# Optimization experiments

Hardware: AMD Instinct MI355X
Metric: run time of the kernel (lower is better)

Reference implementation:

```python
import jax, jax.numpy as jnp
import numpy as np

N_NODES = 100000
N_EDGES = 3200000
N_FEAT = 512
N_CLASS = 10
HIDDEN = 16
EPS = 1e-12  # matches torch F.normalize clamp


def setup_inputs() -> dict:
    key = jax.random.key(0)
    ks = jax.random.split(key, 6)
    x = jax.random.normal(ks[0], (N_NODES, N_FEAT), dtype=jnp.float32)
    edge_index = jax.random.randint(ks[1], (2, N_EDGES), 0, N_NODES, dtype=jnp.int64)
    W1 = jax.random.normal(ks[2], (N_FEAT, HIDDEN), dtype=jnp.float32) / np.sqrt(N_FEAT)
    b1 = jnp.zeros((HIDDEN,), dtype=jnp.float32)
    beta = jnp.ones((1,), dtype=jnp.float32)  # learnable scalar of prop2
    W2 = jax.random.normal(ks[3], (HIDDEN, N_CLASS), dtype=jnp.float32) / np.sqrt(HIDDEN)
    b2 = jnp.zeros((N_CLASS,), dtype=jnp.float32)
    return {"x": x, "edge_index": edge_index, "W1": W1, "b1": b1,
            "beta": beta, "W2": W2, "b2": b2}


def _agnn_conv(h, src, dst, beta_val, n_nodes):
    # L2-normalize node features (cosine attention)
    norm = jnp.maximum(jnp.linalg.norm(h, axis=-1, keepdims=True), EPS)
    hn = h / norm
    # per-edge attention logit: beta * cos(h_i, h_j)
    alpha = beta_val * jnp.sum(hn[src] * hn[dst], axis=-1)  # [E]
    # scatter-softmax over edges sharing the same destination node
    amax = jax.ops.segment_max(alpha, dst, num_segments=n_nodes)
    ea = jnp.exp(alpha - amax[dst])
    denom = jax.ops.segment_sum(ea, dst, num_segments=n_nodes)
    w = ea / denom[dst]  # self-loops guarantee denom > 0
    # weighted aggregation of source features into destination nodes
    return jax.ops.segment_sum(w[:, None] * h[src], dst, num_segments=n_nodes)


def reference(x, edge_index, W1, b1, beta, W2, b2):
    n = x.shape[0]
    # dropout is identity in eval mode
    h = jax.nn.relu(x @ W1 + b1)  # [N, 16]
    # AGNNConv adds self-loops before propagation
    loops = jnp.arange(n, dtype=edge_index.dtype)
    src = jnp.concatenate([edge_index[0], loops])
    dst = jnp.concatenate([edge_index[1], loops])
    h = _agnn_conv(h, src, dst, jnp.float32(1.0), n)   # prop1: beta fixed to 1
    h = _agnn_conv(h, src, dst, beta[0], n)            # prop2: learnable beta
    logits = h @ W2 + b2
    return jax.nn.log_softmax(logits, axis=-1)
```

## Files before the change

kernel.cpp:

```cpp
#include <hip/hip_runtime.h>
#include <hip/hip_fp16.h>
#include <math.h>

#define N_NODES 100000
#define N_EDGES 3200000
#define EPRIME  (N_EDGES + N_NODES)
#define NFEAT   512
#define HID     16
#define NCLS    10

#define NPB     256
#define NB      ((N_NODES + NPB - 1) / NPB)
#define CHUNK   4096
#define NCH     ((EPRIME + CHUNK - 1) / CHUNK)
#define CAPB    10240

union U2 { unsigned int u; __half2 h; };
__device__ __forceinline__ float2 u2f(unsigned int v) {
  U2 t; t.u = v; return __half22float2(t.h);
}

__global__ __launch_bounds__(256) void k_gemm_norm(const float* __restrict__ x,
                                                   const float* __restrict__ W1,
                                                   const float* __restrict__ b1,
                                                   __half* __restrict__ hn1,
                                                   float* __restrict__ norms1,
                                                   int* __restrict__ gcur) {
  if (blockIdx.x == 0)
    for (int i = threadIdx.x; i < NB; i += 256) gcur[i] = 0;

  const int lane = threadIdx.x & 63;
  const int wid  = blockIdx.x * 4 + (threadIdx.x >> 6);
  const int nw   = gridDim.x * 4;

  float4 w[8][4];
#pragma unroll
  for (int kk = 0; kk < 8; ++kk)
#pragma unroll
    for (int j = 0; j < 4; ++j)
      w[kk][j] = *reinterpret_cast<const float4*>(W1 + (lane * 8 + kk) * 16 + j * 4);

  const int outCol = (lane >> 2) & 15;
  const float bias = b1[outCol];

  const float4 z4 = make_float4(0.f, 0.f, 0.f, 0.f);
  float4 c0 = z4, c1 = z4, p0 = z4, p1 = z4, t0 = z4, t1 = z4;

  if (wid < N_NODES) {
    c0 = *reinterpret_cast<const float4*>(x + (size_t)wid * NFEAT + lane * 8);
    c1 = *reinterpret_cast<const float4*>(x + (size_t)wid * NFEAT + lane * 8 + 4);
  }
  if (wid + nw < N_NODES) {
    p0 = *reinterpret_cast<const float4*>(x + (size_t)(wid + nw) * NFEAT + lane * 8);
    p1 = *reinterpret_cast<const float4*>(x + (size_t)(wid + nw) * NFEAT + lane * 8 + 4);
  }

  for (int row = wid; row < N_NODES; row += nw) {
    const int r2 = row + 2 * nw;
    if (r2 < N_NODES) {
      t0 = *reinterpret_cast<const float4*>(x + (size_t)r2 * NFEAT + lane * 8);
      t1 = *reinterpret_cast<const float4*>(x + (size_t)r2 * NFEAT + lane * 8 + 4);
    }

    float xs[8] = {c0.x, c0.y, c0.z, c0.w, c1.x, c1.y, c1.z, c1.w};

    float acc[16];
#pragma unroll
    for (int j = 0; j < 16; ++j) acc[j] = 0.f;

#pragma unroll
    for (int kk = 0; kk < 8; ++kk) {
      const float xv = xs[kk];
#pragma unroll
      for (int j4 = 0; j4 < 4; ++j4) {
        acc[j4 * 4 + 0] = fmaf(xv, w[kk][j4].x, acc[j4 * 4 + 0]);
        acc[j4 * 4 + 1] = fmaf(xv, w[kk][j4].y, acc[j4 * 4 + 1]);
        acc[j4 * 4 + 2] = fmaf(xv, w[kk][j4].z, acc[j4 * 4 + 2]);
        acc[j4 * 4 + 3] = fmaf(xv, w[kk][j4].w, acc[j4 * 4 + 3]);
      }
    }

#pragma unroll
    for (int i = 0; i < 8; ++i) {
      float send = (lane & 32) ? acc[i] : acc[i + 8];
      float r = __shfl_xor(send, 32);
      acc[i] = ((lane & 32) ? acc[i + 8] : acc[i]) + r;
    }
#pragma unroll
    for (int i = 0; i < 4; ++i) {
      float send = (lane & 16) ? acc[i] : acc[i + 4];
      float r = __shfl_xor(send, 16);
      acc[i] = ((lane & 16) ? acc[i + 4] : acc[i]) + r;
    }
#pragma unroll
    for (int i = 0; i < 2; ++i) {
      float send = (lane & 8) ? acc[i] : acc[i + 2];
      float r = __shfl_xor(send, 8);
      acc[i] = ((lane & 8) ? acc[i + 2] : acc[i]) + r;
    }
    {
      float send = (lane & 4) ? acc[0] : acc[1];
      float r = __shfl_xor(send, 4);
      acc[0] = ((lane & 4) ? acc[1] : acc[0]) + r;
    }
    acc[0] += __shfl_xor(acc[0], 2);
    acc[0] += __shfl_xor(acc[0], 1);

    const float v = fmaxf(acc[0] + bias, 0.f);
    float ss = v * v;
    ss += __shfl_xor(ss, 4);
    ss += __shfl_xor(ss, 8);
    ss += __shfl_xor(ss, 16);
    ss += __shfl_xor(ss, 32);
    const float nrm = sqrtf(ss);
    const float vs = v / fmaxf(nrm, 1e-12f);

    const float wv = __shfl(vs, (lane & 15) * 4);
    if (lane < 16) hn1[(size_t)row * HID + lane] = __float2half_rn(wv);
    if (lane == 0) norms1[row] = nrm;

    c0 = p0; c1 = p1; p0 = t0; p1 = t1;
  }
}

__global__ __launch_bounds__(256) void k_part(const int* __restrict__ ei,
                                              int* __restrict__ gcur,
                                              unsigned int* __restrict__ slots) {
  __shared__ int sh_hist[NB];
  __shared__ int sh_gbase[NB];
  const int tid = threadIdx.x;

  for (int i = tid; i < NB; i += 256) sh_hist[i] = 0;
  __syncthreads();

  const int base = blockIdx.x * CHUNK;
  unsigned int pk[16];
  int bk[16], rk[16];
#pragma unroll
  for (int j = 0; j < 16; ++j) {
    int e = base + j * 256 + tid;
    bool valid = (e < EPRIME);
    int srcv = 0, d = 0;
    if (valid) {
      if (e < N_EDGES) { srcv = ei[e]; d = ei[N_EDGES + e]; }
      else             { srcv = d = e - N_EDGES; }
    }
    bk[j] = valid ? (d >> 8) : -1;
    pk[j] = (unsigned)srcv | ((unsigned)(d & 255) << 20);
    rk[j] = valid ? atomicAdd(&sh_hist[d >> 8], 1) : 0;
  }
  __syncthreads();

  for (int i = tid; i < NB; i += 256) {
    int hc = sh_hist[i];
    sh_gbase[i] = hc ? atomicAdd(&gcur[i], hc) : 0;
  }
  __syncthreads();

#pragma unroll
  for (int j = 0; j < 16; ++j)
    if (bk[j] >= 0)
      slots[(size_t)bk[j] * CAPB + sh_gbase[bk[j]] + rk[j]] = pk[j];
}

__global__ __launch_bounds__(256) void k_csr(const unsigned int* __restrict__ slots,
                                             const int* __restrict__ gcur,
                                             unsigned int* __restrict__ csr,
                                             unsigned int* __restrict__ soffs,
                                             unsigned short* __restrict__ ecnt) {
  __shared__ int sh_cnt[NPB];
  __shared__ int sh_cnt2[NPB];
  __shared__ int sh_sc[NPB];
  __shared__ int sh_loffs[NPB];
  const int b = blockIdx.x, tid = threadIdx.x;
  const int ne = gcur[b];
  const unsigned int* my = slots + (size_t)b * CAPB;

  sh_cnt[tid] = 0;
  sh_cnt2[tid] = 0;
  __syncthreads();

  for (int i = tid; i < ne; i += 256) atomicAdd(&sh_cnt[my[i] >> 20], 1);
  __syncthreads();

  const int v = sh_cnt[tid];
  sh_sc[tid] = v;
  __syncthreads();
  for (int d = 1; d < NPB; d <<= 1) {
    int u = (tid >= d) ? sh_sc[tid - d] : 0;
    __syncthreads();
    sh_sc[tid] += u;
    __syncthreads();
  }
  const int excl = sh_sc[tid] - v;
  sh_loffs[tid] = excl;

  if (tid < 16) csr[(size_t)b * CAPB + ne + tid] = 0;

  const int node = b * NPB + tid;
  if (node < N_NODES) {
    soffs[node] = (unsigned)(b * CAPB + excl);
    ecnt[node]  = (unsigned short)v;
  }
  __syncthreads();

  for (int i = tid; i < ne; i += 256) {
    const unsigned pv = my[i];
    const int local = pv >> 20;
    const int r = atomicAdd(&sh_cnt2[local], 1);
    csr[(size_t)b * CAPB + sh_loffs[local] + r] = pv & 0xFFFFF;
  }
}

template <bool FINAL>
__device__ __forceinline__ void pull_body(const __half* __restrict__ hn,
                                          const float* __restrict__ norms,
                                          const unsigned int* __restrict__ soffs,
                                          const unsigned short* __restrict__ ecnt,
                                          const unsigned int* __restrict__ csr,
                                          float beta,
                                          __half* __restrict__ out_hn,
                                          float* __restrict__ out_norms,
                                          const float* __restrict__ W2,
                                          const float* __restrict__ b2,
                                          float* __restrict__ out) {
  const int node = blockIdx.x * 4 + (threadIdx.x >> 6);
  if (node >= N_NODES) return;
  const int lane = threadIdx.x & 63;
  const int q    = lane & 3;
  const int slot = lane >> 2;

  float w4x = 0.f, w4y = 0.f, w4z = 0.f, w4w = 0.f, b2v = 0.f;
  if (FINAL) {
    const int sc = (slot < NCLS) ? slot : 0;
    w4x = W2[(q * 4 + 0) * NCLS + sc];
    w4y = W2[(q * 4 + 1) * NCLS + sc];
    w4z = W2[(q * 4 + 2) * NCLS + sc];
    w4w = W2[(q * 4 + 3) * NCLS + sc];
    b2v = b2[sc];
  }

  const uint2 qraw = *reinterpret_cast<const uint2*>(hn + (size_t)node * HID + q * 4);
  const float2 qa = u2f(qraw.x), qb = u2f(qraw.y);
  const unsigned s = soffs[node];
  const unsigned e = s + ecnt[node];

  float den = 0.f;
  float ax = 0.f, ay = 0.f, az = 0.f, aw = 0.f;

  for (unsigned bi = s; bi < e; bi += 16) {
    const unsigned i = bi + slot;
    const int src = (int)csr[i];
    const uint2 r = *reinterpret_cast<const uint2*>(hn + (size_t)src * HID + q * 4);
    const float2 f0 = u2f(r.x), f1 = u2f(r.y);
    float pd = qa.x * f0.x + qa.y * f0.y + qb.x * f1.x + qb.y * f1.y;
    pd += __shfl_xor(pd, 1);
    pd += __shfl_xor(pd, 2);
    const float t = (i < e) ? __expf(beta * pd) : 0.f;
    den += t;
    const float wgt = t * norms[src];
    ax += wgt * f0.x; ay += wgt * f0.y; az += wgt * f1.x; aw += wgt * f1.y;
  }

#pragma unroll
  for (int m = 4; m <= 32; m <<= 1) {
    den += __shfl_xor(den, m);
    ax  += __shfl_xor(ax, m);
    ay  += __shfl_xor(ay, m);
    az  += __shfl_xor(az, m);
    aw  += __shfl_xor(aw, m);
  }
  const float inv = 1.0f / den;
  ax *= inv; ay *= inv; az *= inv; aw *= inv;

  if (!FINAL) {
    float ssn = ax * ax + ay * ay + az * az + aw * aw;
    ssn += __shfl_xor(ssn, 1);
    ssn += __shfl_xor(ssn, 2);
    const float nrm = sqrtf(ssn);
    const float ninv = 1.0f / fmaxf(nrm, 1e-12f);
    if (lane < 4) {
      U2 lo, hi;
      lo.h = __floats2half2_rn(ax * ninv, ay * ninv);
      hi.h = __floats2half2_rn(az * ninv, aw * ninv);
      *reinterpret_cast<uint2*>(out_hn + (size_t)node * HID + q * 4) =
          make_uint2(lo.u, hi.u);
      if (lane == 0) out_norms[node] = nrm;
    }
  } else {
    float part = ax * w4x + ay * w4y + az * w4z + aw * w4w;
    part += __shfl_xor(part, 1);
    part += __shfl_xor(part, 2);
    const float logit = part + b2v;

    float lg[NCLS];
#pragma unroll
    for (int c = 0; c < NCLS; ++c) lg[c] = __shfl(logit, c * 4);
    float m = lg[0];
#pragma unroll
    for (int c = 1; c < NCLS; ++c) m = fmaxf(m, lg[c]);
    float se = 0.f;
#pragma unroll
    for (int c = 0; c < NCLS; ++c) se += __expf(lg[c] - m);
    const float ls = m + logf(se);

    const float myv = __shfl(logit, lane * 4);
    if (lane < NCLS) out[(size_t)node * NCLS + lane] = myv - ls;
  }
}

__global__ __launch_bounds__(256) void k_pull1(const __half* __restrict__ hn1,
                                               const float* __restrict__ norms1,
                                               const unsigned int* __restrict__ soffs,
                                               const unsigned short* __restrict__ ecnt,
                                               const unsigned int* __restrict__ csr,
                                               __half* __restrict__ hn2,
                                               float* __restrict__ norms2) {
  pull_body<false>(hn1, norms1, soffs, ecnt, csr, 1.0f, hn2, norms2,
                   nullptr, nullptr, nullptr);
}

__global__ __launch_bounds__(256) void k_pull2(const __half* __restrict__ hn2,
                                               const float* __restrict__ norms2,
                                               const unsigned int* __restrict__ soffs,
                                               const unsigned short* __restrict__ ecnt,
                                               const unsigned int* __restrict__ csr,
                                               const float* __restrict__ beta_ptr,
                                               const float* __restrict__ W2,
                                               const float* __restrict__ b2,
                                               float* __restrict__ out) {
  pull_body<true>(hn2, norms2, soffs, ecnt, csr, beta_ptr[0], nullptr, nullptr,
                  W2, b2, out);
}

extern "C" void kernel_launch(void* const* d_in, const int* in_sizes, int n_in,
                              void* d_out, int out_size, void* d_ws, size_t ws_size,
                              hipStream_t stream) {
  const float* x    = (const float*)d_in[0];
  const int*   ei   = (const int*)d_in[1];
  const float* W1   = (const float*)d_in[2];
  const float* b1   = (const float*)d_in[3];
  const float* beta = (const float*)d_in[4];
  const float* W2   = (const float*)d_in[5];
  const float* b2   = (const float*)d_in[6];
  float* out = (float*)d_out;

  char* p = (char*)d_ws;
  __half* hn1 = (__half*)p;                 p += (size_t)N_NODES * HID * 2;
  float* norms1 = (float*)p;                p += (size_t)N_NODES * 4;
  __half* hn2 = (__half*)p;                 p += (size_t)N_NODES * HID * 2;
  float* norms2 = (float*)p;                p += (size_t)N_NODES * 4;
  unsigned int* soffs = (unsigned int*)p;   p += (size_t)N_NODES * 4;
  unsigned short* ecnt = (unsigned short*)p; p += (size_t)N_NODES * 2 + 64;
  int* gcur = (int*)p;                      p += (size_t)NB * 4 + 32;
  unsigned int* csr = (unsigned int*)p;     p += ((size_t)NB * CAPB + 16) * 4;
  unsigned int* slots = (unsigned int*)p;

  k_gemm_norm<<<1024, 256, 0, stream>>>(x, W1, b1, hn1, norms1, gcur);
  k_part<<<NCH, 256, 0, stream>>>(ei, gcur, slots);
  k_csr<<<NB, 256, 0, stream>>>(slots, gcur, csr, soffs, ecnt);

  const int nblW = (N_NODES + 3) / 4;
  k_pull1<<<nblW, 256, 0, stream>>>(hn1, norms1, soffs, ecnt, csr, hn2, norms2);
  k_pull2<<<nblW, 256, 0, stream>>>(hn2, norms2, soffs, ecnt, csr, beta, W2, b2, out);
}
```

Measured before the change: 260.0 us.

## Split GEMM row across two waves with LDS reduction to cut register pressure

The first-layer GEMM now assigns each 512-wide row to two waves, each holding half of W1 (64 float4 registers instead of 128) and one float4 of x per row. Partial sums are combined through a double-buffered shared-memory array with a block barrier, and one wave computes ReLU, the L2 norm and the fp16 store. The grid doubles to 2048 blocks and launch bounds request 4 blocks per CU, aiming for higher occupancy so this memory-bound pass over x hides more latency. The cost is a __syncthreads per row iteration and less outstanding load data per wave.

```diff
diff --git a/kernel.cpp b/kernel.cpp
--- a/kernel.cpp
+++ b/kernel.cpp
@@ -14,62 +14,65 @@
 #define CHUNK   4096
 #define NCH     ((EPRIME + CHUNK - 1) / CHUNK)
 #define CAPB    10240
+#define GBLK    2048
 
 union U2 { unsigned int u; __half2 h; };
 __device__ __forceinline__ float2 u2f(unsigned int v) {
   U2 t; t.u = v; return __half22float2(t.h);
 }
 
-__global__ __launch_bounds__(256) void k_gemm_norm(const float* __restrict__ x,
-                                                   const float* __restrict__ W1,
-                                                   const float* __restrict__ b1,
-                                                   __half* __restrict__ hn1,
-                                                   float* __restrict__ norms1,
-                                                   int* __restrict__ gcur) {
+__global__ __launch_bounds__(256, 4) void k_gemm_norm(const float* __restrict__ x,
+                                                      const float* __restrict__ W1,
+                                                      const float* __restrict__ b1,
+                                                      __half* __restrict__ hn1,
+                                                      float* __restrict__ norms1,
+                                                      int* __restrict__ gcur) {
   if (blockIdx.x == 0)
     for (int i = threadIdx.x; i < NB; i += 256) gcur[i] = 0;
 
+  __shared__ float red[2][2][2][16];
+
   const int lane = threadIdx.x & 63;
-  const int wid  = blockIdx.x * 4 + (threadIdx.x >> 6);
-  const int nw   = gridDim.x * 4;
-
-  float4 w[8][4];
-#pragma unroll
-  for (int kk = 0; kk < 8; ++kk)
+  const int wv   = threadIdx.x >> 6;
+  const int r    = wv >> 1;
+  const int h    = wv & 1;
+  const int stride = GBLK * 2;
+  const int row0 = blockIdx.x * 2 + r;
+  const int nIter = (N_NODES - 1 - blockIdx.x * 2) / stride + 1;
+
+  float4 w[4][4];
+#pragma unroll
+  for (int kk = 0; kk < 4; ++kk)
 #pragma unroll
     for (int j = 0; j < 4; ++j)
-      w[kk][j] = *reinterpret_cast<const float4*>(W1 + (lane * 8 + kk) * 16 + j * 4);
-
-  const int outCol = (lane >> 2) & 15;
-  const float bias = b1[outCol];
+      w[kk][j] = *reinterpret_cast<const float4*>(
+          W1 + (size_t)(h * 256 + lane * 4 + kk) * 16 + j * 4);
+
+  const float bias = (lane < 16) ? b1[lane] : 0.f;
+  const int koff = h * 256 + lane * 4;
 
   const float4 z4 = make_float4(0.f, 0.f, 0.f, 0.f);
-  float4 c0 = z4, c1 = z4, p0 = z4, p1 = z4, t0 = z4, t1 = z4;
-
-  if (wid < N_NODES) {
-    c0 = *reinterpret_cast<const float4*>(x + (size_t)wid * NFEAT + lane * 8);
-    c1 = *reinterpret_cast<const float4*>(x + (size_t)wid * NFEAT + lane * 8 + 4);
-  }
-  if (wid + nw < N_NODES) {
-    p0 = *reinterpret_cast<const float4*>(x + (size_t)(wid + nw) * NFEAT + lane * 8);
-    p1 = *reinterpret_cast<const float4*>(x + (size_t)(wid + nw) * NFEAT + lane * 8 + 4);
-  }
-
-  for (int row = wid; row < N_NODES; row += nw) {
-    const int r2 = row + 2 * nw;
-    if (r2 < N_NODES) {
-      t0 = *reinterpret_cast<const float4*>(x + (size_t)r2 * NFEAT + lane * 8);
-      t1 = *reinterpret_cast<const float4*>(x + (size_t)r2 * NFEAT + lane * 8 + 4);
-    }
-
-    float xs[8] = {c0.x, c0.y, c0.z, c0.w, c1.x, c1.y, c1.z, c1.w};
+  float4 c0 = z4, p0 = z4, t0 = z4;
+
+  if (row0 < N_NODES)
+    c0 = *reinterpret_cast<const float4*>(x + (size_t)row0 * NFEAT + koff);
+  if (row0 + stride < N_NODES)
+    p0 = *reinterpret_cast<const float4*>(x + (size_t)(row0 + stride) * NFEAT + koff);
+
+  for (int i = 0; i < nIter; ++i) {
+    const int row = row0 + i * stride;
+    const int r2 = row + 2 * stride;
+    if (r2 < N_NODES)
+      t0 = *reinterpret_cast<const float4*>(x + (size_t)r2 * NFEAT + koff);
+
+    const float xs[4] = {c0.x, c0.y, c0.z, c0.w};
 
     float acc[16];
 #pragma unroll
     for (int j = 0; j < 16; ++j) acc[j] = 0.f;
 
 #pragma unroll
-    for (int kk = 0; kk < 8; ++kk) {
+    for (int kk = 0; kk < 4; ++kk) {
       const float xv = xs[kk];
 #pragma unroll
       for (int j4 = 0; j4 < 4; ++j4) {
@@ -81,45 +84,50 @@
     }
 
 #pragma unroll
-    for (int i = 0; i < 8; ++i) {
-      float send = (lane & 32) ? acc[i] : acc[i + 8];
-      float r = __shfl_xor(send, 32);
-      acc[i] = ((lane & 32) ? acc[i + 8] : acc[i]) + r;
-    }
-#pragma unroll
-    for (int i = 0; i < 4; ++i) {
-      float send = (lane & 16) ? acc[i] : acc[i + 4];
-      float r = __shfl_xor(send, 16);
-      acc[i] = ((lane & 16) ? acc[i + 4] : acc[i]) + r;
-    }
-#pragma unroll
-    for (int i = 0; i < 2; ++i) {
-      float send = (lane & 8) ? acc[i] : acc[i + 2];
-      float r = __shfl_xor(send, 8);
-      acc[i] = ((lane & 8) ? acc[i + 2] : acc[i]) + r;
+    for (int j = 0; j < 8; ++j) {
+      float send = (lane & 32) ? acc[j] : acc[j + 8];
+      float rr = __shfl_xor(send, 32);
+      acc[j] = ((lane & 32) ? acc[j + 8] : acc[j]) + rr;
+    }
+#pragma unroll
+    for (int j = 0; j < 4; ++j) {
+      float send = (lane & 16) ? acc[j] : acc[j + 4];
+      float rr = __shfl_xor(send, 16);
+      acc[j] = ((lane & 16) ? acc[j + 4] : acc[j]) + rr;
+    }
+#pragma unroll
+    for (int j = 0; j < 2; ++j) {
+      float send = (lane & 8) ? acc[j] : acc[j + 2];
+      float rr = __shfl_xor(send, 8);
+      acc[j] = ((lane & 8) ? acc[j + 2] : acc[j]) + rr;
     }
     {
       float send = (lane & 4) ? acc[0] : acc[1];
-      float r = __shfl_xor(send, 4);
-      acc[0] = ((lane & 4) ? acc[1] : acc[0]) + r;
+      float rr = __shfl_xor(send, 4);
+      acc[0] = ((lane & 4) ? acc[1] : acc[0]) + rr;
     }
     acc[0] += __shfl_xor(acc[0], 2);
     acc[0] += __shfl_xor(acc[0], 1);
 
-    const float v = fmaxf(acc[0] + bias, 0.f);
-    float ss = v * v;
-    ss += __shfl_xor(ss, 4);
-    ss += __shfl_xor(ss, 8);
-    ss += __shfl_xor(ss, 16);
-    ss += __shfl_xor(ss, 32);
-    const float nrm = sqrtf(ss);
-    const float vs = v / fmaxf(nrm, 1e-12f);
-
-    const float wv = __shfl(vs, (lane & 15) * 4);
-    if (lane < 16) hn1[(size_t)row * HID + lane] = __float2half_rn(wv);
-    if (lane == 0) norms1[row] = nrm;
-
-    c0 = p0; c1 = p1; p0 = t0; p1 = t1;
+    if ((lane & 3) == 0) red[i & 1][r][h][lane >> 2] = acc[0];
+    __syncthreads();
+
+    if (h == 0 && row < N_NODES) {
+      float v = 0.f;
+      if (lane < 16)
+        v = fmaxf(red[i & 1][r][0][lane] + red[i & 1][r][1][lane] + bias, 0.f);
+      float ss = v * v;
+      ss += __shfl_xor(ss, 1);
+      ss += __shfl_xor(ss, 2);
+      ss += __shfl_xor(ss, 4);
+      ss += __shfl_xor(ss, 8);
+      const float nrm = sqrtf(ss);
+      const float inv = 1.0f / fmaxf(nrm, 1e-12f);
+      if (lane < 16) hn1[(size_t)row * HID + lane] = __float2half_rn(v * inv);
+      if (lane == 0) norms1[row] = nrm;
+    }
+
+    c0 = p0; p0 = t0;
   }
 }
 
@@ -207,8 +215,8 @@
   for (int i = tid; i < ne; i += 256) {
     const unsigned pv = my[i];
     const int local = pv >> 20;
-    const int r = atomicAdd(&sh_cnt2[local], 1);
-    csr[(size_t)b * CAPB + sh_loffs[local] + r] = pv & 0xFFFFF;
+    const int rr = atomicAdd(&sh_cnt2[local], 1);
+    csr[(size_t)b * CAPB + sh_loffs[local] + rr] = pv & 0xFFFFF;
   }
 }
 
@@ -251,8 +259,8 @@
   for (unsigned bi = s; bi < e; bi += 16) {
     const unsigned i = bi + slot;
     const int src = (int)csr[i];
-    const uint2 r = *reinterpret_cast<const uint2*>(hn + (size_t)src * HID + q * 4);
-    const float2 f0 = u2f(r.x), f1 = u2f(r.y);
+    const uint2 rr = *reinterpret_cast<const uint2*>(hn + (size_t)src * HID + q * 4);
+    const float2 f0 = u2f(rr.x), f1 = u2f(rr.y);
     float pd = qa.x * f0.x + qa.y * f0.y + qb.x * f1.x + qb.y * f1.y;
     pd += __shfl_xor(pd, 1);
     pd += __shfl_xor(pd, 2);
@@ -356,7 +364,7 @@
   unsigned int* csr = (unsigned int*)p;     p += ((size_t)NB * CAPB + 16) * 4;
   unsigned int* slots = (unsigned int*)p;
 
-  k_gemm_norm<<<1024, 256, 0, stream>>>(x, W1, b1, hn1, norms1, gcur);
+  k_gemm_norm<<<GBLK, 256, 0, stream>>>(x, W1, b1, hn1, norms1, gcur);
   k_part<<<NCH, 256, 0, stream>>>(ei, gcur, slots);
   k_csr<<<NB, 256, 0, stream>>>(slots, gcur, csr, soffs, ecnt);
 
```

After: 260.0 us. No clear change (-0.0%).
